# Optimization experiments

Hardware: AMD Instinct MI355X
Metric: run time of the kernel (lower is better)

The kernel has to match this reference:

```python
import jax, jax.numpy as jnp
import numpy as np

N, E, G = 50000, 800000, 64
F_IN, HID = 128, 128


def setup_inputs() -> dict:
    key = jax.random.key(0)
    ks = jax.random.split(key, 8)
    x = jax.random.normal(ks[0], (N, F_IN), dtype=jnp.float32)
    edge_index = jax.random.randint(ks[1], (2, E), 0, N, dtype=jnp.int32)
    batch = jnp.sort(jax.random.randint(ks[2], (N,), 0, G, dtype=jnp.int32))
    def glorot(k, shape):
        fan = shape[0] + shape[1]
        return jax.random.normal(k, shape, dtype=jnp.float32) * jnp.sqrt(2.0 / fan)
    return {
        "x": x,
        "edge_index": edge_index,
        "batch": batch,
        "W0": glorot(ks[3], (F_IN, HID)), "b0": jnp.zeros((HID,), jnp.float32),
        "W1": glorot(ks[4], (HID, HID)), "b1": jnp.zeros((HID,), jnp.float32),
        "W2": glorot(ks[5], (HID, HID)), "b2": jnp.zeros((HID,), jnp.float32),
        "fcW": glorot(ks[6], (HID, 1)), "fcb": jnp.zeros((1,), jnp.float32),
    }


def _gcn_graph_norm(edge_index, n):
    # add self loops, compute symmetric normalization D^-1/2 (A+I) D^-1/2
    loop = jnp.arange(n, dtype=edge_index.dtype)
    src = jnp.concatenate([edge_index[0], loop])
    dst = jnp.concatenate([edge_index[1], loop])
    deg = jax.ops.segment_sum(jnp.ones_like(dst, dtype=jnp.float32), dst, num_segments=n)
    dis = jnp.where(deg > 0, jax.lax.rsqrt(jnp.maximum(deg, 1.0)), 0.0)
    norm = dis[src] * dis[dst]  # [E+N]
    return src, dst, norm


def _gcn_conv(x, W, b, src, dst, norm, n):
    h = x @ W                                 # [N, H] dense transform first (cheaper)
    msg = h[src] * norm[:, None]              # gather + scale  [E+N, H]
    out = jax.ops.segment_sum(msg, dst, num_segments=n)  # scatter-add
    return out + b


def reference(x, edge_index, batch, W0, b0, W1, b1, W2, b2, fcW, fcb):
    n = x.shape[0]
    src, dst, norm = _gcn_graph_norm(edge_index, n)
    h = _gcn_conv(x, W0, b0, src, dst, norm, n)
    h = jax.nn.relu(h)  # dropout is identity in eval mode
    h = _gcn_conv(h, W1, b1, src, dst, norm, n)
    h = jax.nn.relu(h)
    h = _gcn_conv(h, W2, b2, src, dst, norm, n)
    # global mean pool over graphs
    sums = jax.ops.segment_sum(h, batch, num_segments=G)          # [G, H]
    cnts = jax.ops.segment_sum(jnp.ones((n,), jnp.float32), batch, num_segments=G)
    pooled = sums / jnp.maximum(cnts, 1.0)[:, None]
    return (pooled @ fcW + fcb).squeeze(-1)  # [G]
```

## Files before the change

kernel.cpp:

```cpp
#include <hip/hip_runtime.h>
#include <hip/hip_bf16.h>
#include <hip/hip_fp16.h>

#define NTHREADS 256
#define GTHREADS 512
#define POOL_CHUNK 32
#define BKT_EDGES 4096
#define CAP 8192

typedef __attribute__((ext_vector_type(8))) short short8;
typedef __attribute__((ext_vector_type(4))) float f32x4;

__device__ __forceinline__ unsigned short f32_bf16(float f) {
  unsigned u = __float_as_uint(f);
  u += 0x7FFF + ((u >> 16) & 1);
  return (unsigned short)(u >> 16);
}
__device__ __forceinline__ float bf16_f32(unsigned short h) {
  return __uint_as_float((unsigned)h << 16);
}


__global__ __launch_bounds__(NTHREADS) void cursor_init_kernel(int* __restrict__ cursor, int NB) {
  int b = threadIdx.x;
  if (b < NB) cursor[b] = b * CAP;
}


__global__ __launch_bounds__(NTHREADS) void bucketize_kernel(
    const int* __restrict__ src, const int* __restrict__ dst,
    int* __restrict__ cursor, unsigned* __restrict__ store, int E) {
  __shared__ unsigned packed[BKT_EDGES];
  __shared__ unsigned char bkt[BKT_EDGES];
  __shared__ int hist[256];
  __shared__ int base[256];
  const int tid = threadIdx.x;
  const int e0 = blockIdx.x * BKT_EDGES;
  const int cnt = min(BKT_EDGES, E - e0);

  hist[tid] = 0;
  __syncthreads();
  for (int i = tid; i < cnt; i += NTHREADS) {
    int s = src[e0 + i];
    int d = dst[e0 + i];
    packed[i] = ((unsigned)s << 8) | (unsigned)(d & 255);
    int b = d >> 8;
    bkt[i] = (unsigned char)b;
    atomicAdd(&hist[b], 1);
  }
  __syncthreads();
  int h = hist[tid];
  if (h) base[tid] = atomicAdd(&cursor[tid], h);
  __syncthreads();
  hist[tid] = 0;
  __syncthreads();
  for (int i = tid; i < cnt; i += NTHREADS) {
    int b = bkt[i];
    int off = atomicAdd(&hist[b], 1);
    int pos = base[b] + off;
    if (pos < (b + 1) * CAP) store[pos] = packed[i];
  }
}


__global__ __launch_bounds__(NTHREADS) void bucket_scan_kernel(
    const int* __restrict__ cursor, int* __restrict__ bbase, int NB) {
  __shared__ int v[256];
  int t = threadIdx.x;
  int c = (t < NB) ? (cursor[t] - t * CAP) : 0;
  v[t] = c;
  __syncthreads();
  for (int off = 1; off < 256; off <<= 1) {
    int u = (t >= off) ? v[t - off] : 0;
    __syncthreads();
    v[t] += u;
    __syncthreads();
  }
  if (t < NB) bbase[t] = v[t] - c;
}


__global__ __launch_bounds__(NTHREADS) void build_kernel(
    const unsigned* __restrict__ store, const int* __restrict__ cursor,
    const int* __restrict__ bbase, int* __restrict__ rowptr,
    int* __restrict__ csr_src, float* __restrict__ dis, int n, int E, int NB) {
  __shared__ unsigned eb[CAP];
  __shared__ unsigned ord[CAP];
  __shared__ int hist[256];
  __shared__ int scn[256];
  __shared__ int eoff[256];
  const int b = blockIdx.x;
  const int t = threadIdx.x;
  int cnt = min(cursor[b] - b * CAP, CAP);
  const int base = bbase[b];

  for (int i = t; i < cnt; i += NTHREADS) eb[i] = store[(size_t)b * CAP + i];
  hist[t] = 0;
  __syncthreads();
  for (int i = t; i < cnt; i += NTHREADS) atomicAdd(&hist[eb[i] & 255u], 1);
  __syncthreads();

  const int node = b * 256 + t;
  const int deg = hist[t];
  if (node < n) dis[node] = rsqrtf((float)deg + 1.0f);

  scn[t] = deg;
  __syncthreads();
  for (int off = 1; off < 256; off <<= 1) {
    int u = (t >= off) ? scn[t - off] : 0;
    __syncthreads();
    scn[t] += u;
    __syncthreads();
  }
  int excl = scn[t] - deg;
  eoff[t] = excl;
  if (node <= n) rowptr[node] = base + excl;
  if (b == NB - 1 && t == 255) rowptr[n] = E;
  __syncthreads();
  hist[t] = 0;
  __syncthreads();
  for (int i = t; i < cnt; i += NTHREADS) {
    unsigned p = eb[i];
    int dl = p & 255u;
    int off = atomicAdd(&hist[dl], 1);
    ord[eoff[dl] + off] = p >> 8;
  }
  __syncthreads();
  for (int i = t; i < cnt; i += NTHREADS) csr_src[base + i] = (int)ord[i];
}


__global__ __launch_bounds__(128) void bounds_kernel(
    const int* __restrict__ batch, int* __restrict__ gstart, int n, int G) {
  int g = blockIdx.x * blockDim.x + threadIdx.x;
  if (g > G) return;
  int lo = 0, hi = n;
  while (lo < hi) {
    int mid = (lo + hi) >> 1;
    if (batch[mid] < g) lo = mid + 1; else hi = mid;
  }
  gstart[g] = lo;
}


__global__ __launch_bounds__(NTHREADS) void prep_w_kernel(
    const float* __restrict__ W0, const float* __restrict__ W1,
    const float* __restrict__ W2, unsigned short* __restrict__ wt_hi,
    unsigned short* __restrict__ wt_lo) {
  int idx = blockIdx.x * NTHREADS + threadIdx.x;
  int w = idx >> 14;
  int e = idx & 16383;
  int c = e >> 7, k = e & 127;
  const float* W = (w == 0) ? W0 : ((w == 1) ? W1 : W2);
  float v = W[k * 128 + c];
  unsigned short hi = f32_bf16(v);
  unsigned short lo = f32_bf16(v - bf16_f32(hi));
  size_t off = (size_t)w * 16384 + (k >> 3) * 1024 + c * 8 + (k & 7);
  wt_hi[off] = hi;
  wt_lo[off] = lo;
}


template <bool BF16_IN>
__global__ __launch_bounds__(GTHREADS) void gemm_mfma_kernel(
    const void* __restrict__ in_, const unsigned short* __restrict__ wt_hi,
    const unsigned short* __restrict__ wt_lo, const float* __restrict__ dis,
    __half* __restrict__ hs, int n) {
  __shared__ unsigned short Whi[16384];
  __shared__ unsigned short Wlo[16384];
  const int tid = threadIdx.x;
  const int wave = tid >> 6, lane = tid & 63;
  const int g = lane >> 4, lr = lane & 15;

#pragma unroll
  for (int i = 0; i < 4; ++i) {
    int c = i * GTHREADS + tid;
    ((short8*)Whi)[c] = ((const short8*)wt_hi)[c];
    ((short8*)Wlo)[c] = ((const short8*)wt_lo)[c];
  }

  const int rowbase = blockIdx.x * 128 + wave * 16;
  const int arow = rowbase + lr;
  const int arow_c = (arow < n) ? arow : (n - 1);

  short8 a[4];
  if (BF16_IN) {
    const unsigned short* in = (const unsigned short*)in_;
#pragma unroll
    for (int ks = 0; ks < 4; ++ks) {
      union { short8 v; unsigned short u[8]; } t;
      t.v = *(const short8*)&in[(size_t)arow_c * 128 + ks * 32 + g * 8];
#pragma unroll
      for (int i = 0; i < 8; ++i) t.u[i] = (t.u[i] & 0x8000) ? 0 : t.u[i];
      a[ks] = t.v;
    }
  } else {
    const float* in = (const float*)in_;
#pragma unroll
    for (int ks = 0; ks < 4; ++ks) {
      union { short8 v; unsigned short u[8]; } t;
      const float* p = &in[(size_t)arow_c * 128 + ks * 32 + g * 8];
#pragma unroll
      for (int i = 0; i < 8; ++i) t.u[i] = f32_bf16(p[i]);
      a[ks] = t.v;
    }
  }

  __syncthreads();

  f32x4 acc[8];
#pragma unroll
  for (int ct = 0; ct < 8; ++ct) acc[ct] = (f32x4){0.f, 0.f, 0.f, 0.f};

#pragma unroll
  for (int ks = 0; ks < 4; ++ks) {
    const int kb = (ks * 4 + g) * 1024 + lr * 8;
    short8 bf[8];
#pragma unroll
    for (int ct = 0; ct < 8; ++ct) bf[ct] = *(const short8*)&Whi[kb + ct * 128];
#pragma unroll
    for (int ct = 0; ct < 8; ++ct)
      acc[ct] = __builtin_amdgcn_mfma_f32_16x16x32_bf16(a[ks], bf[ct], acc[ct], 0, 0, 0);
#pragma unroll
    for (int ct = 0; ct < 8; ++ct) bf[ct] = *(const short8*)&Wlo[kb + ct * 128];
#pragma unroll
    for (int ct = 0; ct < 8; ++ct)
      acc[ct] = __builtin_amdgcn_mfma_f32_16x16x32_bf16(a[ks], bf[ct], acc[ct], 0, 0, 0);
  }

  float dsv[4];
  int orow[4];
#pragma unroll
  for (int r = 0; r < 4; ++r) {
    orow[r] = rowbase + g * 4 + r;
    dsv[r] = (orow[r] < n) ? dis[orow[r]] : 0.f;
  }
#pragma unroll
  for (int ct = 0; ct < 8; ++ct) {
    int col = ct * 16 + lr;
#pragma unroll
    for (int r = 0; r < 4; ++r) {
      if (orow[r] < n)
        hs[(size_t)orow[r] * 128 + col] = __float2half(acc[ct][r] * dsv[r]);
    }
  }
}


__global__ __launch_bounds__(NTHREADS) void agg_kernel(
    const __half2* __restrict__ hs, const int* __restrict__ rowptr,
    const int* __restrict__ csr_src, const float* __restrict__ dis,
    const float* __restrict__ b, unsigned* __restrict__ out, int n) {
  int node = blockIdx.x * (NTHREADS / 64) + (threadIdx.x >> 6);
  int lane = threadIdx.x & 63;
  if (node >= n) return;
  int r0 = rowptr[node];
  int r1 = rowptr[node + 1];
  float di = dis[node];
  const char* hsb = (const char*)hs + lane * 4;

  float2 acc = __half22float2(hs[(size_t)node * 64 + lane]);
  float2 acc2 = make_float2(0.f, 0.f);
  float2 acc3 = make_float2(0.f, 0.f);
  float2 acc4 = make_float2(0.f, 0.f);

  int e = r0;
  for (; e + 15 < r1; e += 16) {
    int s[16];
#pragma unroll
    for (int j = 0; j < 16; ++j) s[j] = csr_src[e + j];
    __half2 v[16];
#pragma unroll
    for (int j = 0; j < 16; ++j)
      v[j] = *(const __half2*)(hsb + ((unsigned)s[j] << 8));
#pragma unroll
    for (int j = 0; j < 16; j += 4) {
      float2 f0 = __half22float2(v[j]);
      float2 f1 = __half22float2(v[j + 1]);
      float2 f2 = __half22float2(v[j + 2]);
      float2 f3 = __half22float2(v[j + 3]);
      acc.x += f0.x; acc.y += f0.y;
      acc2.x += f1.x; acc2.y += f1.y;
      acc3.x += f2.x; acc3.y += f2.y;
      acc4.x += f3.x; acc4.y += f3.y;
    }
  }
  for (; e + 3 < r1; e += 4) {
    int s0 = csr_src[e], s1 = csr_src[e + 1], s2 = csr_src[e + 2], s3 = csr_src[e + 3];
    float2 f0 = __half22float2(*(const __half2*)(hsb + ((unsigned)s0 << 8)));
    float2 f1 = __half22float2(*(const __half2*)(hsb + ((unsigned)s1 << 8)));
    float2 f2 = __half22float2(*(const __half2*)(hsb + ((unsigned)s2 << 8)));
    float2 f3 = __half22float2(*(const __half2*)(hsb + ((unsigned)s3 << 8)));
    acc.x += f0.x; acc.y += f0.y;
    acc2.x += f1.x; acc2.y += f1.y;
    acc3.x += f2.x; acc3.y += f2.y;
    acc4.x += f3.x; acc4.y += f3.y;
  }
  for (; e < r1; ++e) {
    int s0 = csr_src[e];
    float2 f0 = __half22float2(*(const __half2*)(hsb + ((unsigned)s0 << 8)));
    acc.x += f0.x; acc.y += f0.y;
  }
  acc.x += acc2.x + acc3.x + acc4.x;
  acc.y += acc2.y + acc3.y + acc4.y;

  float2 bb = *(const float2*)&b[lane * 2];
  float rx = fmaf(acc.x, di, bb.x);
  float ry = fmaf(acc.y, di, bb.y);
  unsigned lo = f32_bf16(rx);
  unsigned hi = f32_bf16(ry);
  out[(size_t)node * 64 + lane] = lo | (hi << 16);
}


__global__ __launch_bounds__(NTHREADS) void pool_kernel(
    const unsigned* __restrict__ h, const int* __restrict__ batch,
    float* __restrict__ sums, int n) {
  int wid = blockIdx.x * (NTHREADS / 64) + (threadIdx.x >> 6);
  int lane = threadIdx.x & 63;
  int i0 = wid * POOL_CHUNK;
  if (i0 >= n) return;
  int i1 = min(i0 + POOL_CHUNK, n);

  int g = batch[i0];
  float2 acc = make_float2(0.f, 0.f);
  for (int i = i0; i < i1; ++i) {
    int gi = batch[i];
    if (gi != g) {
      float* sp = &sums[g * 128 + lane * 2];
      atomicAdd(sp, acc.x);
      atomicAdd(sp + 1, acc.y);
      acc = make_float2(0.f, 0.f);
      g = gi;
    }
    unsigned v = h[(size_t)i * 64 + lane];
    acc.x += __uint_as_float(v << 16);
    acc.y += __uint_as_float(v & 0xFFFF0000u);
  }
  float* sp = &sums[g * 128 + lane * 2];
  atomicAdd(sp, acc.x);
  atomicAdd(sp + 1, acc.y);
}


__global__ __launch_bounds__(64) void fc_kernel(
    const float* __restrict__ sums, const int* __restrict__ gstart,
    const float* __restrict__ fcW, const float* __restrict__ fcb,
    float* __restrict__ out) {
  int g = blockIdx.x;
  int lane = threadIdx.x;
  float2 v = *(const float2*)&sums[g * 128 + lane * 2];
  float2 w = *(const float2*)&fcW[lane * 2];
  float p = v.x * w.x + v.y * w.y;
#pragma unroll
  for (int off = 32; off > 0; off >>= 1) p += __shfl_down(p, off);
  if (lane == 0) {
    float c = (float)(gstart[g + 1] - gstart[g]);
    out[g] = p / fmaxf(c, 1.0f) + fcb[0];
  }
}

extern "C" void kernel_launch(void* const* d_in, const int* in_sizes, int n_in,
                              void* d_out, int out_size, void* d_ws, size_t ws_size,
                              hipStream_t stream) {
  const float* x   = (const float*)d_in[0];
  const int* eidx  = (const int*)d_in[1];
  const int* batch = (const int*)d_in[2];
  const float* W0  = (const float*)d_in[3];
  const float* b0  = (const float*)d_in[4];
  const float* W1  = (const float*)d_in[5];
  const float* b1  = (const float*)d_in[6];
  const float* W2  = (const float*)d_in[7];
  const float* b2  = (const float*)d_in[8];
  const float* fcW = (const float*)d_in[9];
  const float* fcb = (const float*)d_in[10];
  float* out = (float*)d_out;

  const int N = in_sizes[0] / 128;
  const int E = in_sizes[1] / 2;
  const int G = out_size;
  const int NB = (N + 255) >> 8;

  const int* src = eidx;
  const int* dst = eidx + E;

  char* ws = (char*)d_ws;
  size_t off = 0;
  auto alloc = [&](size_t bytes) {
    void* p = ws + off;
    off = (off + bytes + 255) & ~(size_t)255;
    return p;
  };
  float*          dis    = (float*)         alloc((size_t)N * 4);
  int*            rowptr = (int*)           alloc((size_t)(N + 1) * 4);
  int*            cursor = (int*)           alloc((size_t)NB * 4);
  int*            bbase  = (int*)           alloc((size_t)NB * 4);
  int*            csrsrc = (int*)           alloc((size_t)E * 4);
  unsigned*       store  = (unsigned*)      alloc((size_t)NB * CAP * 4);
  __half*         hsbuf  = (__half*)        alloc((size_t)N * 128 * 2);
  unsigned*       bufA   = (unsigned*)      alloc((size_t)N * 64 * 4);
  unsigned short* wt_hi  = (unsigned short*)alloc((size_t)3 * 16384 * 2);
  unsigned short* wt_lo  = (unsigned short*)alloc((size_t)3 * 16384 * 2);
  float*          sums   = (float*)         alloc((size_t)G * 128 * 4);
  int*            gstart = (int*)           alloc((size_t)(G + 1) * 4);

  hipMemsetAsync(sums, 0, (size_t)G * 128 * sizeof(float), stream);

  prep_w_kernel<<<192, NTHREADS, 0, stream>>>(W0, W1, W2, wt_hi, wt_lo);
  cursor_init_kernel<<<1, NTHREADS, 0, stream>>>(cursor, NB);
  bucketize_kernel<<<(E + BKT_EDGES - 1) / BKT_EDGES, NTHREADS, 0, stream>>>(
      src, dst, cursor, store, E);
  bucket_scan_kernel<<<1, NTHREADS, 0, stream>>>(cursor, bbase, NB);
  build_kernel<<<NB, NTHREADS, 0, stream>>>(
      store, cursor, bbase, rowptr, csrsrc, dis, N, E, NB);
  bounds_kernel<<<1, 128, 0, stream>>>(batch, gstart, N, G);

  const int gemm_blocks = (N + 127) / 128;
  const int node_blocks = (N + 3) / 4;

  gemm_mfma_kernel<false><<<gemm_blocks, GTHREADS, 0, stream>>>(
      x, wt_hi, wt_lo, dis, hsbuf, N);
  agg_kernel<<<node_blocks, NTHREADS, 0, stream>>>(
      (const __half2*)hsbuf, rowptr, csrsrc, dis, b0, bufA, N);
  gemm_mfma_kernel<true><<<gemm_blocks, GTHREADS, 0, stream>>>(
      bufA, wt_hi + 16384, wt_lo + 16384, dis, hsbuf, N);
  agg_kernel<<<node_blocks, NTHREADS, 0, stream>>>(
      (const __half2*)hsbuf, rowptr, csrsrc, dis, b1, bufA, N);
  gemm_mfma_kernel<true><<<gemm_blocks, GTHREADS, 0, stream>>>(
      bufA, wt_hi + 32768, wt_lo + 32768, dis, hsbuf, N);
  agg_kernel<<<node_blocks, NTHREADS, 0, stream>>>(
      (const __half2*)hsbuf, rowptr, csrsrc, dis, b2, bufA, N);

  const int pool_waves = (N + POOL_CHUNK - 1) / POOL_CHUNK;
  pool_kernel<<<(pool_waves + 3) / 4, NTHREADS, 0, stream>>>(bufA, batch, sums, N);
  fc_kernel<<<G, 64, 0, stream>>>(sums, gstart, fcW, fcb, out);
}
```

Measured before the change: 205.0 us.

## Store hidden features in column-sliced layout so aggregation gathers fit in cache

Hidden features move from row-major [N,128] to eight slices of 16 columns each ([8][N][16]), in both the GEMM output and the aggregation output. The aggregation kernel launches one block per node group and slice, so each slice (about 1.6 MB in fp16) can stay resident in L2 while the random gathers run. Within a wave, eight lanes cover the 16 columns and eight edges are processed in parallel, then combined with shuffles. The cost is 32-byte gather granularity, eight times more reads of rowptr and csr_src, and narrower stores. The GEMM input loads and the pool kernel change to the new layout.

```diff
diff --git a/kernel.cpp b/kernel.cpp
--- a/kernel.cpp
+++ b/kernel.cpp
@@ -185,11 +185,13 @@
 
   short8 a[4];
   if (BF16_IN) {
-    const unsigned short* in = (const unsigned short*)in_;
+    const char* inb = (const char*)in_;
+    const size_t sstride = (size_t)n * 32;
 #pragma unroll
     for (int ks = 0; ks < 4; ++ks) {
       union { short8 v; unsigned short u[8]; } t;
-      t.v = *(const short8*)&in[(size_t)arow_c * 128 + ks * 32 + g * 8];
+      int slice = ks * 2 + (g >> 1);
+      t.v = *(const short8*)(inb + (size_t)slice * sstride + (size_t)arow_c * 32 + (g & 1) * 16);
 #pragma unroll
       for (int i = 0; i < 8; ++i) t.u[i] = (t.u[i] & 0x8000) ? 0 : t.u[i];
       a[ks] = t.v;
@@ -235,81 +237,55 @@
     orow[r] = rowbase + g * 4 + r;
     dsv[r] = (orow[r] < n) ? dis[orow[r]] : 0.f;
   }
+  const size_t n16 = (size_t)n * 16;
 #pragma unroll
   for (int ct = 0; ct < 8; ++ct) {
-    int col = ct * 16 + lr;
 #pragma unroll
     for (int r = 0; r < 4; ++r) {
       if (orow[r] < n)
-        hs[(size_t)orow[r] * 128 + col] = __float2half(acc[ct][r] * dsv[r]);
+        hs[(size_t)ct * n16 + (size_t)orow[r] * 16 + lr] =
+            __float2half(acc[ct][r] * dsv[r]);
     }
   }
 }
 
 
 __global__ __launch_bounds__(NTHREADS) void agg_kernel(
-    const __half2* __restrict__ hs, const int* __restrict__ rowptr,
+    const __half* __restrict__ hs_t, const int* __restrict__ rowptr,
     const int* __restrict__ csr_src, const float* __restrict__ dis,
-    const float* __restrict__ b, unsigned* __restrict__ out, int n) {
-  int node = blockIdx.x * (NTHREADS / 64) + (threadIdx.x >> 6);
-  int lane = threadIdx.x & 63;
+    const float* __restrict__ b, unsigned* __restrict__ out_t, int n) {
+  const int slice = blockIdx.x & 7;
+  const int group = blockIdx.x >> 3;
+  const int wave = threadIdx.x >> 6, lane = threadIdx.x & 63;
+  const int node = group * (NTHREADS / 64) + wave;
   if (node >= n) return;
-  int r0 = rowptr[node];
-  int r1 = rowptr[node + 1];
-  float di = dis[node];
-  const char* hsb = (const char*)hs + lane * 4;
-
-  float2 acc = __half22float2(hs[(size_t)node * 64 + lane]);
-  float2 acc2 = make_float2(0.f, 0.f);
-  float2 acc3 = make_float2(0.f, 0.f);
-  float2 acc4 = make_float2(0.f, 0.f);
-
-  int e = r0;
-  for (; e + 15 < r1; e += 16) {
-    int s[16];
-#pragma unroll
-    for (int j = 0; j < 16; ++j) s[j] = csr_src[e + j];
-    __half2 v[16];
-#pragma unroll
-    for (int j = 0; j < 16; ++j)
-      v[j] = *(const __half2*)(hsb + ((unsigned)s[j] << 8));
-#pragma unroll
-    for (int j = 0; j < 16; j += 4) {
-      float2 f0 = __half22float2(v[j]);
-      float2 f1 = __half22float2(v[j + 1]);
-      float2 f2 = __half22float2(v[j + 2]);
-      float2 f3 = __half22float2(v[j + 3]);
-      acc.x += f0.x; acc.y += f0.y;
-      acc2.x += f1.x; acc2.y += f1.y;
-      acc3.x += f2.x; acc3.y += f2.y;
-      acc4.x += f3.x; acc4.y += f3.y;
-    }
-  }
-  for (; e + 3 < r1; e += 4) {
-    int s0 = csr_src[e], s1 = csr_src[e + 1], s2 = csr_src[e + 2], s3 = csr_src[e + 3];
-    float2 f0 = __half22float2(*(const __half2*)(hsb + ((unsigned)s0 << 8)));
-    float2 f1 = __half22float2(*(const __half2*)(hsb + ((unsigned)s1 << 8)));
-    float2 f2 = __half22float2(*(const __half2*)(hsb + ((unsigned)s2 << 8)));
-    float2 f3 = __half22float2(*(const __half2*)(hsb + ((unsigned)s3 << 8)));
-    acc.x += f0.x; acc.y += f0.y;
-    acc2.x += f1.x; acc2.y += f1.y;
-    acc3.x += f2.x; acc3.y += f2.y;
-    acc4.x += f3.x; acc4.y += f3.y;
-  }
-  for (; e < r1; ++e) {
-    int s0 = csr_src[e];
-    float2 f0 = __half22float2(*(const __half2*)(hsb + ((unsigned)s0 << 8)));
-    acc.x += f0.x; acc.y += f0.y;
-  }
-  acc.x += acc2.x + acc3.x + acc4.x;
-  acc.y += acc2.y + acc3.y + acc4.y;
-
-  float2 bb = *(const float2*)&b[lane * 2];
-  float rx = fmaf(acc.x, di, bb.x);
-  float ry = fmaf(acc.y, di, bb.y);
-  unsigned lo = f32_bf16(rx);
-  unsigned hi = f32_bf16(ry);
-  out[(size_t)node * 64 + lane] = lo | (hi << 16);
+  const int c = lane & 7, es = lane >> 3;
+  const __half* hsl = hs_t + (size_t)slice * n * 16;
+  const int r0 = rowptr[node], r1 = rowptr[node + 1];
+  const float di = dis[node];
+
+  float2 acc = make_float2(0.f, 0.f);
+  if (es == 0)
+    acc = __half22float2(*(const __half2*)(hsl + (size_t)node * 16 + c * 2));
+
+  for (int e = r0 + es; e < r1; e += 8) {
+    int s = csr_src[e];
+    float2 f = __half22float2(*(const __half2*)(hsl + (size_t)s * 16 + c * 2));
+    acc.x += f.x;
+    acc.y += f.y;
+  }
+
+  acc.x += __shfl_down(acc.x, 32); acc.y += __shfl_down(acc.y, 32);
+  acc.x += __shfl_down(acc.x, 16); acc.y += __shfl_down(acc.y, 16);
+  acc.x += __shfl_down(acc.x, 8);  acc.y += __shfl_down(acc.y, 8);
+
+  if (lane < 8) {
+    float2 bb = *(const float2*)&b[slice * 16 + lane * 2];
+    float rx = fmaf(acc.x, di, bb.x);
+    float ry = fmaf(acc.y, di, bb.y);
+    out_t[(size_t)slice * n * 8 + (size_t)node * 8 + lane] =
+        (unsigned)f32_bf16(rx) | ((unsigned)f32_bf16(ry) << 16);
+  }
 }
 
 
@@ -322,22 +298,25 @@
   if (i0 >= n) return;
   int i1 = min(i0 + POOL_CHUNK, n);
 
+  const unsigned* hsl = h + (size_t)(lane >> 3) * n * 8 + (lane & 7);
+  const int col = (lane >> 3) * 16 + (lane & 7) * 2;
+
   int g = batch[i0];
   float2 acc = make_float2(0.f, 0.f);
   for (int i = i0; i < i1; ++i) {
     int gi = batch[i];
     if (gi != g) {
-      float* sp = &sums[g * 128 + lane * 2];
+      float* sp = &sums[g * 128 + col];
       atomicAdd(sp, acc.x);
       atomicAdd(sp + 1, acc.y);
       acc = make_float2(0.f, 0.f);
       g = gi;
     }
-    unsigned v = h[(size_t)i * 64 + lane];
+    unsigned v = hsl[(size_t)i * 8];
     acc.x += __uint_as_float(v << 16);
     acc.y += __uint_as_float(v & 0xFFFF0000u);
   }
-  float* sp = &sums[g * 128 + lane * 2];
+  float* sp = &sums[g * 128 + col];
   atomicAdd(sp, acc.x);
   atomicAdd(sp + 1, acc.y);
 }
@@ -416,22 +395,22 @@
   bounds_kernel<<<1, 128, 0, stream>>>(batch, gstart, N, G);
 
   const int gemm_blocks = (N + 127) / 128;
-  const int node_blocks = (N + 3) / 4;
+  const int agg_blocks = ((N + 3) / 4) * 8;
+  const int pool_waves = (N + POOL_CHUNK - 1) / POOL_CHUNK;
 
   gemm_mfma_kernel<false><<<gemm_blocks, GTHREADS, 0, stream>>>(
       x, wt_hi, wt_lo, dis, hsbuf, N);
-  agg_kernel<<<node_blocks, NTHREADS, 0, stream>>>(
-      (const __half2*)hsbuf, rowptr, csrsrc, dis, b0, bufA, N);
+  agg_kernel<<<agg_blocks, NTHREADS, 0, stream>>>(
+      hsbuf, rowptr, csrsrc, dis, b0, bufA, N);
   gemm_mfma_kernel<true><<<gemm_blocks, GTHREADS, 0, stream>>>(
       bufA, wt_hi + 16384, wt_lo + 16384, dis, hsbuf, N);
-  agg_kernel<<<node_blocks, NTHREADS, 0, stream>>>(
-      (const __half2*)hsbuf, rowptr, csrsrc, dis, b1, bufA, N);
+  agg_kernel<<<agg_blocks, NTHREADS, 0, stream>>>(
+      hsbuf, rowptr, csrsrc, dis, b1, bufA, N);
   gemm_mfma_kernel<true><<<gemm_blocks, GTHREADS, 0, stream>>>(
       bufA, wt_hi + 32768, wt_lo + 32768, dis, hsbuf, N);
-  agg_kernel<<<node_blocks, NTHREADS, 0, stream>>>(
-      (const __half2*)hsbuf, rowptr, csrsrc, dis, b2, bufA, N);
-
-  const int pool_waves = (N + POOL_CHUNK - 1) / POOL_CHUNK;
+  agg_kernel<<<agg_blocks, NTHREADS, 0, stream>>>(
+      hsbuf, rowptr, csrsrc, dis, b2, bufA, N);
+
   pool_kernel<<<(pool_waves + 3) / 4, NTHREADS, 0, stream>>>(bufA, batch, sums, N);
   fc_kernel<<<G, 64, 0, stream>>>(sums, gstart, fcW, fcb, out);
 }
```

Result: slower. 437.4 us (+113.3%).
